# Performance work log

Hardware: AMD Instinct MI355X
Metric: run time of the kernel (lower is better)

## Reference

```python
import jax, jax.numpy as jnp
import numpy as np

B, T, D, H, L = 16, 1500, 512, 1024, 20


def setup_inputs() -> dict:
    key = jax.random.key(0)
    ks = jax.random.split(key, 5)
    return {
        "x": jax.random.normal(ks[0], (B, T, D), dtype=jnp.float32),
        "w1": jax.random.normal(ks[1], (D, H), dtype=jnp.float32) * (1.0 / np.sqrt(D)),
        "b1": jax.random.normal(ks[2], (H,), dtype=jnp.float32) * 0.01,
        "wp": jax.random.normal(ks[3], (H, D), dtype=jnp.float32) * (1.0 / np.sqrt(H)),
        "wa": jax.random.normal(ks[4], (D, L), dtype=jnp.float32) * (1.0 / np.sqrt(D)),
    }


def reference(x, w1, b1, wp, wa):
    # x: [B,T,D]
    f1 = jax.nn.relu(x @ w1 + b1)          # [B,T,H]
    p1 = f1 @ wp                            # [B,T,D] (output_dim == input_dim)
    lorder = wa.shape[1]
    t = p1.shape[1]
    # left-pad time axis with lorder-1 zeros so shift i looks at p1[t-i]
    padded = jnp.pad(p1, ((0, 0), (lorder - 1, 0), (0, 0)))  # [B,T+L-1,D]
    # z[..., i] = p1 shifted back by i frames (zero for t-i < 0)
    z = jnp.stack(
        [jax.lax.dynamic_slice_in_dim(padded, lorder - 1 - i, t, axis=1)
         for i in range(lorder)],
        axis=-1,
    )  # [B,T,D,L]
    att = jax.nn.softmax(x @ wa, axis=-1)   # [B,T,L]
    out1 = jnp.einsum('btdl,btl->btd', z, att)
    return x + out1
```

## Files before the change

kernel.cpp:

```cpp
#include <hip/hip_runtime.h>
#include <hip/hip_bf16.h>

#define Bd 16
#define Td 1500
#define Dd 512
#define Hd 1024
#define Ld 20
#define Md (Bd*Td)

using f32x4  = __attribute__((ext_vector_type(4))) float;
using short8 = __attribute__((ext_vector_type(8))) short;

__device__ __forceinline__ unsigned short f2bf(float f) {
    union { float f; unsigned u; } v; v.f = f;
    unsigned r = v.u + 0x7fffu + ((v.u >> 16) & 1u);
    return (unsigned short)(r >> 16);
}
__device__ __forceinline__ float bf2f(unsigned short u) {
    union { unsigned u; float f; } v; v.u = ((unsigned)u) << 16;
    return v.f;
}
__device__ __forceinline__ void gload_lds16(const void* g, void* l) {
    __builtin_amdgcn_global_load_lds(
        (const __attribute__((address_space(1))) unsigned*)g,
        (__attribute__((address_space(3))) unsigned*)l, 16, 0, 0);
}

__global__ __launch_bounds__(256) void cvt_x_kernel(
    const float* __restrict__ in, unsigned short* __restrict__ out)
{
    size_t i = ((size_t)blockIdx.x * 256 + threadIdx.x) * 8;
    float4 v0 = *(const float4*)(in + i);
    float4 v1 = *(const float4*)(in + i + 4);
    union { unsigned short us[8]; int4 v; } p;
    p.us[0] = f2bf(v0.x); p.us[1] = f2bf(v0.y); p.us[2] = f2bf(v0.z); p.us[3] = f2bf(v0.w);
    p.us[4] = f2bf(v1.x); p.us[5] = f2bf(v1.y); p.us[6] = f2bf(v1.z); p.us[7] = f2bf(v1.w);
    *(int4*)(out + i) = p.v;
}

__global__ __launch_bounds__(256) void transpose_convert_k(
    const float* __restrict__ W, unsigned short* __restrict__ WT, int K, int N)
{
    __shared__ float tile[32][33];
    int n0 = blockIdx.x * 32, k0 = blockIdx.y * 32;
    int tx = threadIdx.x, ty = threadIdx.y;
#pragma unroll
    for (int j = 0; j < 32; j += 8)
        tile[ty + j][tx] = W[(size_t)(k0 + ty + j) * N + n0 + tx];
    __syncthreads();
#pragma unroll
    for (int j = 0; j < 32; j += 8)
        WT[(size_t)(n0 + ty + j) * K + k0 + tx] = f2bf(tile[tx][ty + j]);
}

__global__ __launch_bounds__(256) void prep_waT_kernel(
    const float* __restrict__ wa, unsigned short* __restrict__ waT)
{
    int i = blockIdx.x * 256 + threadIdx.x;
    int c = i >> 9, d = i & 511;
    waT[i] = (c < Ld) ? f2bf(wa[(size_t)d * Ld + c]) : (unsigned short)0;
}

template<bool RELU_BIAS>
__global__ __launch_bounds__(256) void gemm_lds(
    const unsigned short* __restrict__ A, const unsigned short* __restrict__ BT,
    const float* __restrict__ bias, unsigned short* __restrict__ C,
    int Mdim, int Ndim, int Kdim)
{
    __shared__ __align__(16) unsigned short As[2 * 128 * 32];
    __shared__ __align__(16) unsigned short Bs[2 * 128 * 32];

    const int tid  = threadIdx.x;
    const int lane = tid & 63;
    const int wave = tid >> 6;
    const int wr   = wave >> 1, wc = wave & 1;

    const int nx  = gridDim.x;
    const int nwg = nx * gridDim.y;
    const int id  = blockIdx.y * nx + blockIdx.x;
    const int nid = (id & 7) * (nwg >> 3) + (id >> 3);
    const int m0  = (nid / nx) * 128;
    const int n0  = (nid % nx) * 128;

    const int srow  = tid >> 2;
    const int sslot = (tid & 3) ^ ((tid >> 3) & 3);
    int ar0 = m0 + srow;      if (ar0 >= Mdim) ar0 = Mdim - 1;
    int ar1 = m0 + 64 + srow; if (ar1 >= Mdim) ar1 = Mdim - 1;
    const unsigned short* a0p = A  + (size_t)ar0 * Kdim + sslot * 8;
    const unsigned short* a1p = A  + (size_t)ar1 * Kdim + sslot * 8;
    const unsigned short* b0p = BT + (size_t)(n0 + srow) * Kdim + sslot * 8;
    const unsigned short* b1p = BT + (size_t)(n0 + 64 + srow) * Kdim + sslot * 8;

    const int rsel = lane & 15;
    const int koff = ((lane >> 4) ^ ((lane >> 1) & 3)) * 8;

    f32x4 acc[4][4] = {};

    const int NT = Kdim >> 5;

    gload_lds16(a0p, As + wave * 512);
    gload_lds16(a1p, As + 2048 + wave * 512);
    gload_lds16(b0p, Bs + wave * 512);
    gload_lds16(b1p, Bs + 2048 + wave * 512);
    __syncthreads();

    for (int t = 0; t < NT; ++t) {
        const int cur = t & 1;
        if (t + 1 < NT) {
            const int kk = (t + 1) * 32;
            unsigned short* as = As + (cur ^ 1) * 4096;
            unsigned short* bs = Bs + (cur ^ 1) * 4096;
            gload_lds16(a0p + kk, as + wave * 512);
            gload_lds16(a1p + kk, as + 2048 + wave * 512);
            gload_lds16(b0p + kk, bs + wave * 512);
            gload_lds16(b1p + kk, bs + 2048 + wave * 512);
        }
        const unsigned short* as = As + cur * 4096;
        const unsigned short* bs = Bs + cur * 4096;
        short8 af[4], bfr[4];
#pragma unroll
        for (int m = 0; m < 4; ++m)
            af[m] = *(const short8*)&as[(wr * 64 + m * 16 + rsel) * 32 + koff];
#pragma unroll
        for (int n = 0; n < 4; ++n)
            bfr[n] = *(const short8*)&bs[(wc * 64 + n * 16 + rsel) * 32 + koff];
#pragma unroll
        for (int m = 0; m < 4; ++m)
#pragma unroll
            for (int n = 0; n < 4; ++n)
                acc[m][n] = __builtin_amdgcn_mfma_f32_16x16x32_bf16(af[m], bfr[n], acc[m][n], 0, 0, 0);
        __syncthreads();
    }

    const int colBase = n0 + wc * 64;
    const int rowBase = m0 + wr * 64 + ((lane >> 4) << 2);
#pragma unroll
    for (int n = 0; n < 4; ++n) {
        const int col = colBase + n * 16 + (lane & 15);
        float bvs = 0.f;
        if (RELU_BIAS) bvs = bias[col];
#pragma unroll
        for (int m = 0; m < 4; ++m) {
#pragma unroll
            for (int j = 0; j < 4; ++j) {
                const int r = rowBase + m * 16 + j;
                if (r < Mdim) {
                    float v = acc[m][n][j];
                    if (RELU_BIAS) v = fmaxf(v + bvs, 0.f);
                    C[(size_t)r * Ndim + col] = f2bf(v);
                }
            }
        }
    }
}

__global__ __launch_bounds__(256) void att_mfma_kernel(
    const unsigned short* __restrict__ xb, const unsigned short* __restrict__ waT,
    float* __restrict__ att)
{
    __shared__ __align__(16) unsigned short waTs[16 * 1024];
    __shared__ __align__(16) unsigned short As[2 * 128 * 32];
    __shared__ float sS[128][33];

    const int tid  = threadIdx.x;
    const int lane = tid & 63;
    const int wave = tid >> 6;
    const int m0   = blockIdx.x * 128;

    for (int i = tid; i < 2048; i += 256) {
        const int off = i * 8;
        const int kt = off >> 10, c = (off >> 5) & 31, sl = (off >> 3) & 3;
        const int ssl = sl ^ ((c >> 1) & 3);
        *(short8*)&waTs[off] = *(const short8*)&waT[(size_t)c * Dd + kt * 32 + ssl * 8];
    }

    const int srow  = tid >> 2;
    const int sslot = (tid & 3) ^ ((tid >> 3) & 3);
    int ar0 = m0 + srow;      if (ar0 >= Md) ar0 = Md - 1;
    int ar1 = m0 + 64 + srow; if (ar1 >= Md) ar1 = Md - 1;
    const unsigned short* a0p = xb + (size_t)ar0 * Dd + sslot * 8;
    const unsigned short* a1p = xb + (size_t)ar1 * Dd + sslot * 8;

    const int rsel = lane & 15;
    const int koff = ((lane >> 4) ^ ((lane >> 1) & 3)) * 8;

    f32x4 acc[2][2] = {};

    gload_lds16(a0p, As + wave * 512);
    gload_lds16(a1p, As + 2048 + wave * 512);
    __syncthreads();

    for (int t = 0; t < 16; ++t) {
        const int cur = t & 1;
        if (t + 1 < 16) {
            unsigned short* as = As + (cur ^ 1) * 4096;
            gload_lds16(a0p + (t + 1) * 32, as + wave * 512);
            gload_lds16(a1p + (t + 1) * 32, as + 2048 + wave * 512);
        }
        const unsigned short* as = As + cur * 4096;
        short8 af[2], bfr[2];
#pragma unroll
        for (int m = 0; m < 2; ++m)
            af[m] = *(const short8*)&as[(wave * 32 + m * 16 + rsel) * 32 + koff];
#pragma unroll
        for (int n = 0; n < 2; ++n)
            bfr[n] = *(const short8*)&waTs[t * 1024 + (n * 16 + rsel) * 32 + koff];
#pragma unroll
        for (int m = 0; m < 2; ++m)
#pragma unroll
            for (int n = 0; n < 2; ++n)
                acc[m][n] = __builtin_amdgcn_mfma_f32_16x16x32_bf16(af[m], bfr[n], acc[m][n], 0, 0, 0);
        __syncthreads();
    }

    const int r0 = wave * 32 + ((lane >> 4) << 2);
#pragma unroll
    for (int m = 0; m < 2; ++m)
#pragma unroll
        for (int n = 0; n < 2; ++n)
#pragma unroll
            for (int j = 0; j < 4; ++j)
                sS[r0 + m * 16 + j][n * 16 + (lane & 15)] = acc[m][n][j];
    __syncthreads();

    if (tid < 128) {
        const int grow = m0 + tid;
        if (grow < Md) {
            float mx = -1e30f;
#pragma unroll
            for (int l = 0; l < Ld; ++l) mx = fmaxf(mx, sS[tid][l]);
            float e[Ld]; float sum = 0.f;
#pragma unroll
            for (int l = 0; l < Ld; ++l) { e[l] = __expf(sS[tid][l] - mx); sum += e[l]; }
            const float inv = 1.f / sum;
#pragma unroll
            for (int l = 0; l < Ld; ++l)
                att[(size_t)grow * Ld + l] = e[l] * inv;
        }
    }
}

__global__ __launch_bounds__(512) void out_kernel(
    const float* __restrict__ x, const unsigned short* __restrict__ p1,
    const float* __restrict__ att, float* __restrict__ out)
{
    const int bid = blockIdx.x;
    const int nid = (bid & 7) * 375 + (bid >> 3);
    const int wave = threadIdx.x >> 6;
    const int lane = threadIdx.x & 63;
    const int row  = nid * 8 + wave;
    const int t    = row % Td;
    const int d0   = lane * 8;

    float av[Ld];
    const float* ar = att + (size_t)row * Ld;
#pragma unroll
    for (int i = 0; i < Ld; i += 4) {
        float4 v = *(const float4*)(ar + i);
        av[i] = v.x; av[i + 1] = v.y; av[i + 2] = v.z; av[i + 3] = v.w;
    }

    const float* xr = x + (size_t)row * Dd + d0;
    float4 xa = *(const float4*)xr;
    float4 xb4 = *(const float4*)(xr + 4);
    float acc[8] = { xa.x, xa.y, xa.z, xa.w, xb4.x, xb4.y, xb4.z, xb4.w };

    const int imax = (t < Ld - 1) ? t : (Ld - 1);
    const unsigned short* pr = p1 + (size_t)row * Dd + d0;
    for (int i = 0; i <= imax; ++i) {
        const float a = av[i];
        short8 p = *(const short8*)(pr - (size_t)i * Dd);
#pragma unroll
        for (int j = 0; j < 8; ++j) acc[j] += a * bf2f((unsigned short)p[j]);
    }
    float* orow = out + (size_t)row * Dd + d0;
    float4 o0 = { acc[0], acc[1], acc[2], acc[3] };
    float4 o1 = { acc[4], acc[5], acc[6], acc[7] };
    *(float4*)orow       = o0;
    *(float4*)(orow + 4) = o1;
}

extern "C" void kernel_launch(void* const* d_in, const int* in_sizes, int n_in,
                              void* d_out, int out_size, void* d_ws, size_t ws_size,
                              hipStream_t stream)
{
    const float* x  = (const float*)d_in[0];
    const float* w1 = (const float*)d_in[1];
    const float* b1 = (const float*)d_in[2];
    const float* wp = (const float*)d_in[3];
    const float* wa = (const float*)d_in[4];
    float* out = (float*)d_out;

    char* ws = (char*)d_ws;
    unsigned short* xb  = (unsigned short*)ws;  ws += (size_t)Md * Dd * 2;
    unsigned short* w1T = (unsigned short*)ws;  ws += (size_t)Hd * Dd * 2;
    unsigned short* wpT = (unsigned short*)ws;  ws += (size_t)Dd * Hd * 2;
    unsigned short* waT = (unsigned short*)ws;  ws += (size_t)32 * Dd * 2;
    unsigned short* f1  = (unsigned short*)ws;  ws += (size_t)Md * Hd * 2;
    unsigned short* p1  = (unsigned short*)ws;  ws += (size_t)Md * Dd * 2;
    float*          att = (float*)ws;           ws += (size_t)Md * Ld * 4;

    cvt_x_kernel<<<(Md * Dd) / 2048, 256, 0, stream>>>(x, xb);
    transpose_convert_k<<<dim3(Hd / 32, Dd / 32), dim3(32, 8), 0, stream>>>(w1, w1T, Dd, Hd);
    transpose_convert_k<<<dim3(Dd / 32, Hd / 32), dim3(32, 8), 0, stream>>>(wp, wpT, Hd, Dd);
    prep_waT_kernel<<<(32 * Dd) / 256, 256, 0, stream>>>(wa, waT);

    const int mtiles = (Md + 127) / 128;
    att_mfma_kernel<<<mtiles, 256, 0, stream>>>(xb, waT, att);

    gemm_lds<true ><<<dim3(Hd / 128, mtiles), 256, 0, stream>>>(xb, w1T, b1, f1, Md, Hd, Dd);
    gemm_lds<false><<<dim3(Dd / 128, mtiles), 256, 0, stream>>>(f1, wpT, nullptr, p1, Md, Dd, Hd);

    out_kernel<<<Md / 8, 512, 0, stream>>>(x, p1, att, out);
}
```

Baseline: 226.1 us.

## Triple-buffer GEMM loads with vmcnt waits, stage epilogue through LDS, retile attention

The bf16 GEMM moves from a double-buffered loop with two full barriers per K step to a three-stage LDS ring. Each step does a partial vmcnt wait and a single barrier, and MFMA issue priority is raised. The epilogue now writes results into swizzled LDS and stores 16-byte vectors per row instead of scattered 2-byte stores. The attention logits kernel switches to 64-row tiles with the same three-stage ring, giving more blocks and less LDS. The trade-offs are hand-tuned waitcnt assumptions about outstanding load counts and an extra LDS round trip in the epilogue.

```diff
diff --git a/kernel.cpp b/kernel.cpp
--- a/kernel.cpp
+++ b/kernel.cpp
@@ -67,8 +67,7 @@
     const float* __restrict__ bias, unsigned short* __restrict__ C,
     int Mdim, int Ndim, int Kdim)
 {
-    __shared__ __align__(16) unsigned short As[2 * 128 * 32];
-    __shared__ __align__(16) unsigned short Bs[2 * 128 * 32];
+    __shared__ __align__(16) unsigned short SH[2][3][128 * 32];
 
     const int tid  = threadIdx.x;
     const int lane = tid & 63;
@@ -95,28 +94,34 @@
     const int koff = ((lane >> 4) ^ ((lane >> 1) & 3)) * 8;
 
     f32x4 acc[4][4] = {};
-
     const int NT = Kdim >> 5;
 
-    gload_lds16(a0p, As + wave * 512);
-    gload_lds16(a1p, As + 2048 + wave * 512);
-    gload_lds16(b0p, Bs + wave * 512);
-    gload_lds16(b1p, Bs + 2048 + wave * 512);
-    __syncthreads();
-
+    auto stage = [&](int t, int b) {
+        const int kk = t * 32;
+        gload_lds16(a0p + kk, &SH[0][b][wave * 512]);
+        gload_lds16(a1p + kk, &SH[0][b][2048 + wave * 512]);
+        gload_lds16(b0p + kk, &SH[1][b][wave * 512]);
+        gload_lds16(b1p + kk, &SH[1][b][2048 + wave * 512]);
+    };
+
+    stage(0, 0);
+    stage(1, 1);
+
+    int buf = 0;
     for (int t = 0; t < NT; ++t) {
-        const int cur = t & 1;
-        if (t + 1 < NT) {
-            const int kk = (t + 1) * 32;
-            unsigned short* as = As + (cur ^ 1) * 4096;
-            unsigned short* bs = Bs + (cur ^ 1) * 4096;
-            gload_lds16(a0p + kk, as + wave * 512);
-            gload_lds16(a1p + kk, as + 2048 + wave * 512);
-            gload_lds16(b0p + kk, bs + wave * 512);
-            gload_lds16(b1p + kk, bs + 2048 + wave * 512);
-        }
-        const unsigned short* as = As + cur * 4096;
-        const unsigned short* bs = Bs + cur * 4096;
+        if (t + 1 < NT) asm volatile("s_waitcnt vmcnt(4)" ::: "memory");
+        else            asm volatile("s_waitcnt vmcnt(0)" ::: "memory");
+        __builtin_amdgcn_s_barrier();
+        asm volatile("" ::: "memory");
+
+        if (t + 2 < NT) {
+            int nb = buf + 2;
+            if (nb >= 3) nb -= 3;
+            stage(t + 2, nb);
+        }
+
+        const unsigned short* as = &SH[0][buf][0];
+        const unsigned short* bs = &SH[1][buf][0];
         short8 af[4], bfr[4];
 #pragma unroll
         for (int m = 0; m < 4; ++m)
@@ -124,32 +129,51 @@
 #pragma unroll
         for (int n = 0; n < 4; ++n)
             bfr[n] = *(const short8*)&bs[(wc * 64 + n * 16 + rsel) * 32 + koff];
+
+        __builtin_amdgcn_s_setprio(1);
 #pragma unroll
         for (int m = 0; m < 4; ++m)
 #pragma unroll
             for (int n = 0; n < 4; ++n)
                 acc[m][n] = __builtin_amdgcn_mfma_f32_16x16x32_bf16(af[m], bfr[n], acc[m][n], 0, 0, 0);
-        __syncthreads();
-    }
-
-    const int colBase = n0 + wc * 64;
-    const int rowBase = m0 + wr * 64 + ((lane >> 4) << 2);
+        __builtin_amdgcn_s_setprio(0);
+
+        ++buf; if (buf == 3) buf = 0;
+    }
+
+    __syncthreads();
+    unsigned short* Cs = (unsigned short*)SH;
+
+    const int rB = wr * 64 + ((lane >> 4) << 2);
+    const int cB = wc * 64;
 #pragma unroll
     for (int n = 0; n < 4; ++n) {
-        const int col = colBase + n * 16 + (lane & 15);
+        const int col = cB + n * 16 + rsel;
         float bvs = 0.f;
-        if (RELU_BIAS) bvs = bias[col];
+        if (RELU_BIAS) bvs = bias[n0 + col];
+        const int s = col >> 3, e = col & 7;
 #pragma unroll
         for (int m = 0; m < 4; ++m) {
 #pragma unroll
             for (int j = 0; j < 4; ++j) {
-                const int r = rowBase + m * 16 + j;
-                if (r < Mdim) {
-                    float v = acc[m][n][j];
-                    if (RELU_BIAS) v = fmaxf(v + bvs, 0.f);
-                    C[(size_t)r * Ndim + col] = f2bf(v);
-                }
+                const int r = rB + m * 16 + j;
+                float v = acc[m][n][j];
+                if (RELU_BIAS) v = fmaxf(v + bvs, 0.f);
+                Cs[r * 128 + ((s ^ (r & 7)) << 3) + e] = f2bf(v);
             }
+        }
+    }
+    __syncthreads();
+
+    const int row = tid >> 1;
+    const int c0  = (tid & 1) * 64;
+    const int gr  = m0 + row;
+    if (gr < Mdim) {
+#pragma unroll
+        for (int i = 0; i < 8; ++i) {
+            const int s = (c0 >> 3) + i;
+            int4 v = *(const int4*)&Cs[row * 128 + ((s ^ (row & 7)) << 3)];
+            *(int4*)&C[(size_t)gr * Ndim + n0 + c0 + i * 8] = v;
         }
     }
 }
@@ -159,13 +183,13 @@
     float* __restrict__ att)
 {
     __shared__ __align__(16) unsigned short waTs[16 * 1024];
-    __shared__ __align__(16) unsigned short As[2 * 128 * 32];
-    __shared__ float sS[128][33];
+    __shared__ __align__(16) unsigned short As[3][64 * 32];
+    __shared__ float sS[64][21];
 
     const int tid  = threadIdx.x;
     const int lane = tid & 63;
     const int wave = tid >> 6;
-    const int m0   = blockIdx.x * 128;
+    const int m0   = blockIdx.x * 64;
 
     for (int i = tid; i < 2048; i += 256) {
         const int off = i * 8;
@@ -173,70 +197,65 @@
         const int ssl = sl ^ ((c >> 1) & 3);
         *(short8*)&waTs[off] = *(const short8*)&waT[(size_t)c * Dd + kt * 32 + ssl * 8];
     }
+    __syncthreads();
 
     const int srow  = tid >> 2;
     const int sslot = (tid & 3) ^ ((tid >> 3) & 3);
-    int ar0 = m0 + srow;      if (ar0 >= Md) ar0 = Md - 1;
-    int ar1 = m0 + 64 + srow; if (ar1 >= Md) ar1 = Md - 1;
-    const unsigned short* a0p = xb + (size_t)ar0 * Dd + sslot * 8;
-    const unsigned short* a1p = xb + (size_t)ar1 * Dd + sslot * 8;
+    const unsigned short* a0p = xb + (size_t)(m0 + srow) * Dd + sslot * 8;
 
     const int rsel = lane & 15;
     const int koff = ((lane >> 4) ^ ((lane >> 1) & 3)) * 8;
 
-    f32x4 acc[2][2] = {};
-
-    gload_lds16(a0p, As + wave * 512);
-    gload_lds16(a1p, As + 2048 + wave * 512);
-    __syncthreads();
-
+    f32x4 acc[2] = {};
+
+    gload_lds16(a0p, &As[0][wave * 512]);
+    gload_lds16(a0p + 32, &As[1][wave * 512]);
+
+    int buf = 0;
     for (int t = 0; t < 16; ++t) {
-        const int cur = t & 1;
-        if (t + 1 < 16) {
-            unsigned short* as = As + (cur ^ 1) * 4096;
-            gload_lds16(a0p + (t + 1) * 32, as + wave * 512);
-            gload_lds16(a1p + (t + 1) * 32, as + 2048 + wave * 512);
-        }
-        const unsigned short* as = As + cur * 4096;
-        short8 af[2], bfr[2];
-#pragma unroll
-        for (int m = 0; m < 2; ++m)
-            af[m] = *(const short8*)&as[(wave * 32 + m * 16 + rsel) * 32 + koff];
-#pragma unroll
-        for (int n = 0; n < 2; ++n)
-            bfr[n] = *(const short8*)&waTs[t * 1024 + (n * 16 + rsel) * 32 + koff];
-#pragma unroll
-        for (int m = 0; m < 2; ++m)
-#pragma unroll
-            for (int n = 0; n < 2; ++n)
-                acc[m][n] = __builtin_amdgcn_mfma_f32_16x16x32_bf16(af[m], bfr[n], acc[m][n], 0, 0, 0);
-        __syncthreads();
-    }
-
-    const int r0 = wave * 32 + ((lane >> 4) << 2);
-#pragma unroll
-    for (int m = 0; m < 2; ++m)
-#pragma unroll
-        for (int n = 0; n < 2; ++n)
+        if (t < 15) asm volatile("s_waitcnt vmcnt(1)" ::: "memory");
+        else        asm volatile("s_waitcnt vmcnt(0)" ::: "memory");
+        __builtin_amdgcn_s_barrier();
+        asm volatile("" ::: "memory");
+
+        if (t + 2 < 16) {
+            int nb = buf + 2; if (nb >= 3) nb -= 3;
+            gload_lds16(a0p + (t + 2) * 32, &As[nb][wave * 512]);
+        }
+
+        short8 af = *(const short8*)&As[buf][(wave * 16 + rsel) * 32 + koff];
+        short8 b0 = *(const short8*)&waTs[t * 1024 + (rsel) * 32 + koff];
+        short8 b1 = *(const short8*)&waTs[t * 1024 + (16 + rsel) * 32 + koff];
+        acc[0] = __builtin_amdgcn_mfma_f32_16x16x32_bf16(af, b0, acc[0], 0, 0, 0);
+        acc[1] = __builtin_amdgcn_mfma_f32_16x16x32_bf16(af, b1, acc[1], 0, 0, 0);
+
+        ++buf; if (buf == 3) buf = 0;
+    }
+
+    const int r0 = wave * 16 + ((lane >> 4) << 2);
+#pragma unroll
+    for (int n = 0; n < 2; ++n) {
+        const int c = n * 16 + rsel;
+        if (c < 21) {
 #pragma unroll
             for (int j = 0; j < 4; ++j)
-                sS[r0 + m * 16 + j][n * 16 + (lane & 15)] = acc[m][n][j];
-    __syncthreads();
-
-    if (tid < 128) {
+                sS[r0 + j][c] = acc[n][j];
+        }
+    }
+    __syncthreads();
+
+    if (tid < 64) {
+        float mx = -1e30f;
+#pragma unroll
+        for (int l = 0; l < Ld; ++l) mx = fmaxf(mx, sS[tid][l]);
+        float e[Ld]; float sum = 0.f;
+#pragma unroll
+        for (int l = 0; l < Ld; ++l) { e[l] = __expf(sS[tid][l] - mx); sum += e[l]; }
+        const float inv = 1.f / sum;
         const int grow = m0 + tid;
-        if (grow < Md) {
-            float mx = -1e30f;
-#pragma unroll
-            for (int l = 0; l < Ld; ++l) mx = fmaxf(mx, sS[tid][l]);
-            float e[Ld]; float sum = 0.f;
-#pragma unroll
-            for (int l = 0; l < Ld; ++l) { e[l] = __expf(sS[tid][l] - mx); sum += e[l]; }
-            const float inv = 1.f / sum;
-#pragma unroll
-            for (int l = 0; l < Ld; ++l)
-                att[(size_t)grow * Ld + l] = e[l] * inv;
-        }
+#pragma unroll
+        for (int l = 0; l < Ld; ++l)
+            att[(size_t)grow * Ld + l] = e[l] * inv;
     }
 }
 
@@ -305,9 +324,9 @@
     transpose_convert_k<<<dim3(Dd / 32, Hd / 32), dim3(32, 8), 0, stream>>>(wp, wpT, Hd, Dd);
     prep_waT_kernel<<<(32 * Dd) / 256, 256, 0, stream>>>(wa, waT);
 
+    att_mfma_kernel<<<Md / 64, 256, 0, stream>>>(xb, waT, att);
+
     const int mtiles = (Md + 127) / 128;
-    att_mfma_kernel<<<mtiles, 256, 0, stream>>>(xb, waT, att);
-
     gemm_lds<true ><<<dim3(Hd / 128, mtiles), 256, 0, stream>>>(xb, w1T, b1, f1, Md, Hd, Dd);
     gemm_lds<false><<<dim3(Dd / 128, mtiles), 256, 0, stream>>>(f1, wpT, nullptr, p1, Md, Dd, Hd);
 
```

Measured after the change: 226.5 us. About the same (+0.2%).
